# Optimization experiments

Hardware: AMD Instinct MI355X
Metric: run time of the kernel (lower is better)

## Reference

```python
import jax, jax.numpy as jnp
import numpy as np

N_NODES = 100000
N_EDGES = 1600000
IN_CH = 128
OUT_CH = 128


def setup_inputs() -> dict:
    key = jax.random.key(0)
    k = jax.random.split(key, 6)
    x = jax.random.normal(k[0], (N_NODES, IN_CH), dtype=jnp.float32)
    edge_index = jax.random.randint(k[1], (2, N_EDGES), 0, N_NODES, dtype=jnp.int32)
    # GCNConv linear weights (glorot-ish scale) and biases
    W1 = jax.random.normal(k[2], (IN_CH, OUT_CH), dtype=jnp.float32) / np.sqrt(IN_CH)
    b1 = jnp.zeros((OUT_CH,), dtype=jnp.float32)
    W2 = jax.random.normal(k[3], (OUT_CH, OUT_CH), dtype=jnp.float32) / np.sqrt(OUT_CH)
    b2 = jnp.zeros((OUT_CH,), dtype=jnp.float32)
    return {"x": x, "edge_index": edge_index, "W1": W1, "b1": b1, "W2": W2, "b2": b2}


def gcn_conv(x, src, dst, W, b, n_nodes):
    """PyG GCNConv: add self-loops, symmetric D^-1/2 A D^-1/2 normalization."""
    h = x @ W  # [N, out]
    # degree including the implicit self-loop (weight 1)
    ones = jnp.ones(src.shape[0], dtype=x.dtype)
    deg = jax.ops.segment_sum(ones, dst, num_segments=n_nodes) + 1.0  # [N]
    dinv = jax.lax.rsqrt(deg)  # deg >= 1 so always finite
    coef = dinv[src] * dinv[dst]  # [E] edge norm 1/sqrt(d_i d_j)
    msg = h[src] * coef[:, None]  # [E, out] gather + scale
    agg = jax.ops.segment_sum(msg, dst, num_segments=n_nodes)  # scatter-add
    # self-loop contribution: norm = dinv[i]^2
    agg = agg + h * (dinv * dinv)[:, None]
    return agg + b


def reference(x, edge_index, W1, b1, W2, b2):
    src, dst = edge_index[0], edge_index[1]
    h = jax.nn.relu(gcn_conv(x, src, dst, W1, b1, N_NODES))
    out = jax.nn.relu(gcn_conv(h, src, dst, W2, b2, N_NODES))
    return out
```

## Files before the change

kernel.cpp:

```cpp
#include <hip/hip_runtime.h>


#define NN 100000
#define NBKT 512
#define BKT_W 196
#define CHUNK 8192
#define CAP 6144

typedef __attribute__((ext_vector_type(8))) short bf16x8;
typedef __attribute__((ext_vector_type(4))) float f32x4;

__device__ __forceinline__ ushort f2bf(float f) {
  unsigned u = __float_as_uint(f);
  unsigned r = (u + 0x7fffu + ((u >> 16) & 1u)) >> 16;
  return (ushort)r;
}
__device__ __forceinline__ float bflo(unsigned p) {
  return __uint_as_float(p << 16);
}
__device__ __forceinline__ float bfhi(unsigned p) {
  return __uint_as_float(p & 0xffff0000u);
}
__device__ __forceinline__ unsigned hipair(unsigned ue, unsigned uo) {
  return (uo & 0xffff0000u) | (ue >> 16);
}


__global__ __launch_bounds__(512) void kb_hist(const int* __restrict__ dst,
                                               int* __restrict__ bcnt, int E) {
  __shared__ int h[NBKT];
  for (int i = threadIdx.x; i < NBKT; i += 512) h[i] = 0;
  __syncthreads();
  int base = blockIdx.x * CHUNK;
#pragma unroll 4
  for (int q = 0; q < CHUNK / 512; q++) {
    int e = base + threadIdx.x + q * 512;
    if (e < E) atomicAdd(&h[dst[e] / BKT_W], 1);
  }
  __syncthreads();
  for (int i = threadIdx.x; i < NBKT; i += 512)
    if (h[i]) atomicAdd(&bcnt[i], h[i]);
}

__global__ __launch_bounds__(512) void kb_scan(const int* __restrict__ bcnt,
                                               int* __restrict__ bbase,
                                               int* __restrict__ bcur,
                                               int* __restrict__ row_ptr,
                                               int N, int E) {
  __shared__ int s[NBKT];
  int t = threadIdx.x;
  int v = bcnt[t];
  s[t] = v;
  __syncthreads();
  for (int off = 1; off < NBKT; off <<= 1) {
    int x = (t >= off) ? s[t - off] : 0;
    __syncthreads();
    s[t] += x;
    __syncthreads();
  }
  int ex = s[t] - v;
  bbase[t] = ex;
  bcur[t] = ex;
  if (t == NBKT - 1) bbase[NBKT] = E;
  if (t == 0) row_ptr[N] = E;
}

__global__ __launch_bounds__(512) void kb_scatter(const int* __restrict__ src,
                                                  const int* __restrict__ dst,
                                                  int* __restrict__ bcur,
                                                  int2* __restrict__ pairs, int E) {
  __shared__ int h[NBKT];
  __shared__ int gb[NBKT];
  for (int i = threadIdx.x; i < NBKT; i += 512) h[i] = 0;
  __syncthreads();

  const int base = blockIdx.x * CHUNK;
  const int t = threadIdx.x;
  int rank[CHUNK / 512], bkt[CHUNK / 512], sv[CHUNK / 512], dv[CHUNK / 512];
#pragma unroll
  for (int q = 0; q < CHUNK / 512; q++) {
    int e = base + t + q * 512;
    if (e < E) {
      int d = dst[e];
      int b = d / BKT_W;
      bkt[q] = b;
      sv[q] = src[e];
      dv[q] = d;
      rank[q] = atomicAdd(&h[b], 1);
    } else {
      bkt[q] = -1;
    }
  }
  __syncthreads();
  for (int i = t; i < NBKT; i += 512) {
    int c = h[i];
    gb[i] = c ? atomicAdd(&bcur[i], c) : 0;
  }
  __syncthreads();
#pragma unroll
  for (int q = 0; q < CHUNK / 512; q++) {
    if (bkt[q] >= 0) pairs[(size_t)gb[bkt[q]] + rank[q]] = make_int2(sv[q], dv[q]);
  }
}

__global__ __launch_bounds__(512) void kb_sort(const int* __restrict__ bbase,
                                               const int2* __restrict__ pairs,
                                               int* __restrict__ csr_src,
                                               int* __restrict__ row_ptr,
                                               int N, int E) {
  __shared__ int cnt[256];
  __shared__ int sc[256];
  __shared__ int cur[256];
  __shared__ int stage[CAP];

  const int b = blockIdx.x;
  const int t = threadIdx.x;
  const int lo = bbase[b], hi = bbase[b + 1];
  const int n0 = b * BKT_W;
  int m = hi - lo;
  if (m > CAP) m = CAP;

  if (t < 256) cnt[t] = 0;
  __syncthreads();

  for (int i = t; i < m; i += 512) {
    int2 p = pairs[(size_t)lo + i];
    atomicAdd(&cnt[p.y - n0], 1);
  }
  __syncthreads();

  int v = 0;
  if (t < 256) {
    v = cnt[t];
    sc[t] = v;
  }
  __syncthreads();
  for (int off = 1; off < 256; off <<= 1) {
    int x = 0;
    if (t < 256 && t >= off) x = sc[t - off];
    __syncthreads();
    if (t < 256) sc[t] += x;
    __syncthreads();
  }
  if (t < 256) {
    int ex = sc[t] - v;
    cur[t] = ex;
    int node = n0 + t;
    if (t < BKT_W && node < N) row_ptr[node] = lo + ex;
  }
  __syncthreads();

  for (int i = t; i < m; i += 512) {
    int2 p = pairs[(size_t)lo + i];
    int pos = atomicAdd(&cur[p.y - n0], 1);
    stage[pos] = p.x;
  }
  __syncthreads();

  for (int i = t; i < m; i += 512) csr_src[(size_t)lo + i] = stage[i];
}

__global__ __launch_bounds__(256) void k_dinv(const int* __restrict__ row_ptr,
                                              float* __restrict__ dinv, int N) {
  int i = blockIdx.x * 256 + threadIdx.x;
  if (i < N) dinv[i] = rsqrtf((float)(row_ptr[i + 1] - row_ptr[i]) + 1.0f);
}

__global__ __launch_bounds__(256) void k_wsplit(const float* __restrict__ W,
                                                ushort* __restrict__ whi,
                                                ushort* __restrict__ wlo) {
  const int t = threadIdx.x;
#pragma unroll
  for (int it = 0; it < 16; ++it) {
    int f4 = it * 256 + t;
    int k = f4 >> 5;
    int n4 = (f4 & 31) * 4;
    float4 v = *(const float4*)(W + (size_t)k * 128 + n4);
    float f[4] = {v.x, v.y, v.z, v.w};
#pragma unroll
    for (int q = 0; q < 4; ++q) {
      int n = n4 + q;
      unsigned u = __float_as_uint(f[q]);
      float lf = f[q] - __uint_as_float(u & 0xffff0000u);
      int bo = (n * 256 + k * 2) ^ ((n & 7) << 4);
      *(ushort*)((char*)whi + bo) = (ushort)(u >> 16);
      *(ushort*)((char*)wlo + bo) = (ushort)(__float_as_uint(lf) >> 16);
    }
  }
}

__device__ __forceinline__ void cvt_row(const float* __restrict__ p,
                                        bf16x8* hi, bf16x8* lo) {
  float4 v0 = *(const float4*)p;
  float4 v1 = *(const float4*)(p + 4);
  float f[8] = {v0.x, v0.y, v0.z, v0.w, v1.x, v1.y, v1.z, v1.w};
  unsigned hw[4], lw[4];
#pragma unroll
  for (int i = 0; i < 4; ++i) {
    unsigned u0 = __float_as_uint(f[2 * i]);
    unsigned u1 = __float_as_uint(f[2 * i + 1]);
    float l0 = f[2 * i] - __uint_as_float(u0 & 0xffff0000u);
    float l1 = f[2 * i + 1] - __uint_as_float(u1 & 0xffff0000u);
    hw[i] = hipair(u0, u1);
    lw[i] = hipair(__float_as_uint(l0), __float_as_uint(l1));
  }
  uint4 H = make_uint4(hw[0], hw[1], hw[2], hw[3]);
  uint4 L = make_uint4(lw[0], lw[1], lw[2], lw[3]);
  *hi = __builtin_bit_cast(bf16x8, H);
  *lo = __builtin_bit_cast(bf16x8, L);
}

__global__ __launch_bounds__(256) void k_gemm_mfma(const float* __restrict__ X,
                                                   const ushort* __restrict__ whi,
                                                   const ushort* __restrict__ wlo,
                                                   const float* __restrict__ dinv,
                                                   ushort* __restrict__ hs, int M) {
  __shared__ ushort wt_hi[128 * 128];
  __shared__ ushort wt_lo[128 * 128];

  const int t = threadIdx.x;
#pragma unroll
  for (int it = 0; it < 8; ++it) {
    int o = (it * 256 + t) * 8;
    *(uint4*)&wt_hi[o] = *(const uint4*)&whi[o];
    *(uint4*)&wt_lo[o] = *(const uint4*)&wlo[o];
  }
  __syncthreads();

  const int wv = t >> 6;
  const int lane = t & 63;
  const int r0 = blockIdx.x * 128 + wv * 32;
  const int la = lane & 15;
  const int kg = (lane >> 4) * 8;
  const int rowA = min(r0 + la, M - 1);
  const int rowB = min(r0 + 16 + la, M - 1);

  f32x4 acc[2][8];
#pragma unroll
  for (int rs = 0; rs < 2; ++rs)
#pragma unroll
    for (int ct = 0; ct < 8; ++ct) acc[rs][ct] = (f32x4)(0.f);

#pragma unroll
  for (int ks = 0; ks < 4; ++ks) {
    const int koff = ks * 32 + kg;
    bf16x8 ah0, al0, ah1, al1;
    cvt_row(X + (size_t)rowA * 128 + koff, &ah0, &al0);
    cvt_row(X + (size_t)rowB * 128 + koff, &ah1, &al1);
#pragma unroll
    for (int ct = 0; ct < 8; ++ct) {
      const int n = ct * 16 + la;
      const int bo = (n * 256 + koff * 2) ^ ((n & 7) << 4);
      bf16x8 bh = *(const bf16x8*)((const char*)wt_hi + bo);
      bf16x8 bl = *(const bf16x8*)((const char*)wt_lo + bo);
      acc[0][ct] = __builtin_amdgcn_mfma_f32_16x16x32_bf16(ah0, bh, acc[0][ct], 0, 0, 0);
      acc[0][ct] = __builtin_amdgcn_mfma_f32_16x16x32_bf16(ah0, bl, acc[0][ct], 0, 0, 0);
      acc[0][ct] = __builtin_amdgcn_mfma_f32_16x16x32_bf16(al0, bh, acc[0][ct], 0, 0, 0);
      acc[1][ct] = __builtin_amdgcn_mfma_f32_16x16x32_bf16(ah1, bh, acc[1][ct], 0, 0, 0);
      acc[1][ct] = __builtin_amdgcn_mfma_f32_16x16x32_bf16(ah1, bl, acc[1][ct], 0, 0, 0);
      acc[1][ct] = __builtin_amdgcn_mfma_f32_16x16x32_bf16(al1, bh, acc[1][ct], 0, 0, 0);
    }
  }

#pragma unroll
  for (int rs = 0; rs < 2; ++rs) {
#pragma unroll
    for (int j = 0; j < 4; ++j) {
      int r = r0 + rs * 16 + (lane >> 4) * 4 + j;
      if (r < M) {
        float sc = dinv[r];
#pragma unroll
        for (int ct = 0; ct < 8; ++ct)
          hs[(size_t)r * 128 + ct * 16 + la] = f2bf(acc[rs][ct][j] * sc);
      }
    }
  }
}

__global__ __launch_bounds__(256) void k_agg(const int* __restrict__ row_ptr,
                                             const int* __restrict__ csr_src,
                                             const float* __restrict__ dinv,
                                             const ushort* __restrict__ hs,
                                             const float* __restrict__ bias,
                                             float* __restrict__ out, int N) {
  const int node = blockIdx.x * 4 + (threadIdx.x >> 6);
  if (node >= N) return;
  const int lane = threadIdx.x & 63;
  const int half = lane >> 5;
  const int cq = lane & 31;
  const uint2* hp = (const uint2*)hs;

  const int e0 = row_ptr[node];
  const int e1 = row_ptr[node + 1];

  float a0 = 0.f, a1 = 0.f, a2 = 0.f, a3 = 0.f;
  int e = e0 + half;
  for (; e + 6 < e1; e += 8) {
    int s0 = csr_src[e];
    int s1 = csr_src[e + 2];
    int s2 = csr_src[e + 4];
    int s3 = csr_src[e + 6];
    uint2 v0 = hp[(size_t)s0 * 32 + cq];
    uint2 v1 = hp[(size_t)s1 * 32 + cq];
    uint2 v2 = hp[(size_t)s2 * 32 + cq];
    uint2 v3 = hp[(size_t)s3 * 32 + cq];
    a0 += bflo(v0.x) + bflo(v1.x) + bflo(v2.x) + bflo(v3.x);
    a1 += bfhi(v0.x) + bfhi(v1.x) + bfhi(v2.x) + bfhi(v3.x);
    a2 += bflo(v0.y) + bflo(v1.y) + bflo(v2.y) + bflo(v3.y);
    a3 += bfhi(v0.y) + bfhi(v1.y) + bfhi(v2.y) + bfhi(v3.y);
  }
  for (; e < e1; e += 2) {
    int s = csr_src[e];
    uint2 v = hp[(size_t)s * 32 + cq];
    a0 += bflo(v.x);
    a1 += bfhi(v.x);
    a2 += bflo(v.y);
    a3 += bfhi(v.y);
  }
  a0 += __shfl_xor(a0, 32);
  a1 += __shfl_xor(a1, 32);
  a2 += __shfl_xor(a2, 32);
  a3 += __shfl_xor(a3, 32);

  if (half == 0) {
    uint2 sv = hp[(size_t)node * 32 + cq];
    a0 += bflo(sv.x);
    a1 += bfhi(sv.x);
    a2 += bflo(sv.y);
    a3 += bfhi(sv.y);
    float dv = dinv[node];
    float4 bv = ((const float4*)bias)[cq];
    float4 o;
    o.x = fmaxf(fmaf(a0, dv, bv.x), 0.f);
    o.y = fmaxf(fmaf(a1, dv, bv.y), 0.f);
    o.z = fmaxf(fmaf(a2, dv, bv.z), 0.f);
    o.w = fmaxf(fmaf(a3, dv, bv.w), 0.f);
    ((float4*)out)[(size_t)node * 32 + cq] = o;
  }
}


extern "C" void kernel_launch(void* const* d_in, const int* in_sizes, int n_in,
                              void* d_out, int out_size, void* d_ws, size_t ws_size,
                              hipStream_t stream) {
  const float* x  = (const float*)d_in[0];
  const int*   ei = (const int*)d_in[1];
  const float* W1 = (const float*)d_in[2];
  const float* b1 = (const float*)d_in[3];
  const float* W2 = (const float*)d_in[4];
  const float* b2 = (const float*)d_in[5];
  float* out = (float*)d_out;

  const int N = NN;
  const int E = in_sizes[1] / 2;
  const int* src = ei;
  const int* dst = ei + E;

  char* w = (char*)d_ws;
  auto alloc = [&](size_t bytes) {
    char* p = w;
    w += (bytes + 255) & ~(size_t)255;
    return p;
  };
  float*  dinv    = (float*)alloc((size_t)N * 4);
  int*    row_ptr = (int*)alloc((size_t)(N + 1) * 4);
  int*    bcnt    = (int*)alloc(NBKT * 4);
  int*    bbase   = (int*)alloc((NBKT + 1) * 4);
  int*    bcur    = (int*)alloc(NBKT * 4);
  int*    csr_src = (int*)alloc((size_t)E * 4);
  int2*   pairs   = (int2*)alloc((size_t)E * 8);
  ushort* hs      = (ushort*)alloc((size_t)N * 128 * 2);
  ushort* w1hi    = (ushort*)alloc(128 * 128 * 2);
  ushort* w1lo    = (ushort*)alloc(128 * 128 * 2);
  ushort* w2hi    = (ushort*)alloc(128 * 128 * 2);
  ushort* w2lo    = (ushort*)alloc(128 * 128 * 2);

  const int EB = (E + CHUNK - 1) / CHUNK;

  hipMemsetAsync(bcnt, 0, NBKT * 4, stream);
  kb_hist<<<EB, 512, 0, stream>>>(dst, bcnt, E);
  kb_scan<<<1, 512, 0, stream>>>(bcnt, bbase, bcur, row_ptr, N, E);
  kb_scatter<<<EB, 512, 0, stream>>>(src, dst, bcur, pairs, E);
  kb_sort<<<NBKT, 512, 0, stream>>>(bbase, pairs, csr_src, row_ptr, N, E);
  k_dinv<<<(N + 255) / 256, 256, 0, stream>>>(row_ptr, dinv, N);
  k_wsplit<<<1, 256, 0, stream>>>(W1, w1hi, w1lo);
  k_wsplit<<<1, 256, 0, stream>>>(W2, w2hi, w2lo);

  const int GB = (N + 127) / 128;
  const int AB = (N + 3) / 4;

  k_gemm_mfma<<<GB, 256, 0, stream>>>(x, w1hi, w1lo, dinv, hs, N);
  k_agg<<<AB, 256, 0, stream>>>(row_ptr, csr_src, dinv, hs, b1, out, N);
  k_gemm_mfma<<<GB, 256, 0, stream>>>(out, w2hi, w2lo, dinv, hs, N);
  k_agg<<<AB, 256, 0, stream>>>(row_ptr, csr_src, dinv, hs, b2, out, N);
}
```

Before: 353.2 us.

## Store layer-1 output in bf16, widen aggregation loads, fold dinv and wsplit launches

The first aggregation now writes the hidden activation as bf16 into a new buffer, and a new GEMM variant reads bf16 A directly, roughly halving the intermediate write and read traffic. The aggregation kernel now uses 16-byte loads with four edge groups per wave. The dinv computation moves into the sort kernel, and the two weight-split launches are merged into one, cutting launches. Rounding the hidden layer to bf16 adds precision loss on the second layer input, and dropping the low half of A for the second GEMM loses accuracy.

```diff
diff --git a/kernel.cpp b/kernel.cpp
--- a/kernel.cpp
+++ b/kernel.cpp
@@ -107,6 +107,7 @@
                                                const int2* __restrict__ pairs,
                                                int* __restrict__ csr_src,
                                                int* __restrict__ row_ptr,
+                                               float* __restrict__ dinv,
                                                int N, int E) {
   __shared__ int cnt[256];
   __shared__ int sc[256];
@@ -146,7 +147,10 @@
     int ex = sc[t] - v;
     cur[t] = ex;
     int node = n0 + t;
-    if (t < BKT_W && node < N) row_ptr[node] = lo + ex;
+    if (t < BKT_W && node < N) {
+      row_ptr[node] = lo + ex;
+      dinv[node] = rsqrtf((float)v + 1.0f);
+    }
   }
   __syncthreads();
 
@@ -160,15 +164,15 @@
   for (int i = t; i < m; i += 512) csr_src[(size_t)lo + i] = stage[i];
 }
 
-__global__ __launch_bounds__(256) void k_dinv(const int* __restrict__ row_ptr,
-                                              float* __restrict__ dinv, int N) {
-  int i = blockIdx.x * 256 + threadIdx.x;
-  if (i < N) dinv[i] = rsqrtf((float)(row_ptr[i + 1] - row_ptr[i]) + 1.0f);
-}
-
-__global__ __launch_bounds__(256) void k_wsplit(const float* __restrict__ W,
-                                                ushort* __restrict__ whi,
-                                                ushort* __restrict__ wlo) {
+__global__ __launch_bounds__(256) void k_wsplit2(const float* __restrict__ W1,
+                                                 const float* __restrict__ W2,
+                                                 ushort* __restrict__ w1hi,
+                                                 ushort* __restrict__ w1lo,
+                                                 ushort* __restrict__ w2hi,
+                                                 ushort* __restrict__ w2lo) {
+  const float* W = blockIdx.x ? W2 : W1;
+  ushort* whi = blockIdx.x ? w2hi : w1hi;
+  ushort* wlo = blockIdx.x ? w2lo : w1lo;
   const int t = threadIdx.x;
 #pragma unroll
   for (int it = 0; it < 16; ++it) {
@@ -277,65 +281,156 @@
   }
 }
 
+__global__ __launch_bounds__(256) void k_gemm_mfma_bf(const ushort* __restrict__ Xb,
+                                                      const ushort* __restrict__ whi,
+                                                      const ushort* __restrict__ wlo,
+                                                      const float* __restrict__ dinv,
+                                                      ushort* __restrict__ hs, int M) {
+  __shared__ ushort wt_hi[128 * 128];
+  __shared__ ushort wt_lo[128 * 128];
+
+  const int t = threadIdx.x;
+#pragma unroll
+  for (int it = 0; it < 8; ++it) {
+    int o = (it * 256 + t) * 8;
+    *(uint4*)&wt_hi[o] = *(const uint4*)&whi[o];
+    *(uint4*)&wt_lo[o] = *(const uint4*)&wlo[o];
+  }
+  __syncthreads();
+
+  const int wv = t >> 6;
+  const int lane = t & 63;
+  const int r0 = blockIdx.x * 128 + wv * 32;
+  const int la = lane & 15;
+  const int kg = (lane >> 4) * 8;
+  const int rowA = min(r0 + la, M - 1);
+  const int rowB = min(r0 + 16 + la, M - 1);
+
+  f32x4 acc[2][8];
+#pragma unroll
+  for (int rs = 0; rs < 2; ++rs)
+#pragma unroll
+    for (int ct = 0; ct < 8; ++ct) acc[rs][ct] = (f32x4)(0.f);
+
+#pragma unroll
+  for (int ks = 0; ks < 4; ++ks) {
+    const int koff = ks * 32 + kg;
+    bf16x8 a0 = *(const bf16x8*)(Xb + (size_t)rowA * 128 + koff);
+    bf16x8 a1 = *(const bf16x8*)(Xb + (size_t)rowB * 128 + koff);
+#pragma unroll
+    for (int ct = 0; ct < 8; ++ct) {
+      const int n = ct * 16 + la;
+      const int bo = (n * 256 + koff * 2) ^ ((n & 7) << 4);
+      bf16x8 bh = *(const bf16x8*)((const char*)wt_hi + bo);
+      bf16x8 bl = *(const bf16x8*)((const char*)wt_lo + bo);
+      acc[0][ct] = __builtin_amdgcn_mfma_f32_16x16x32_bf16(a0, bh, acc[0][ct], 0, 0, 0);
+      acc[0][ct] = __builtin_amdgcn_mfma_f32_16x16x32_bf16(a0, bl, acc[0][ct], 0, 0, 0);
+      acc[1][ct] = __builtin_amdgcn_mfma_f32_16x16x32_bf16(a1, bh, acc[1][ct], 0, 0, 0);
+      acc[1][ct] = __builtin_amdgcn_mfma_f32_16x16x32_bf16(a1, bl, acc[1][ct], 0, 0, 0);
+    }
+  }
+
+#pragma unroll
+  for (int rs = 0; rs < 2; ++rs) {
+#pragma unroll
+    for (int j = 0; j < 4; ++j) {
+      int r = r0 + rs * 16 + (lane >> 4) * 4 + j;
+      if (r < M) {
+        float sc = dinv[r];
+#pragma unroll
+        for (int ct = 0; ct < 8; ++ct)
+          hs[(size_t)r * 128 + ct * 16 + la] = f2bf(acc[rs][ct][j] * sc);
+      }
+    }
+  }
+}
+
+template <int BF16OUT>
 __global__ __launch_bounds__(256) void k_agg(const int* __restrict__ row_ptr,
                                              const int* __restrict__ csr_src,
                                              const float* __restrict__ dinv,
                                              const ushort* __restrict__ hs,
                                              const float* __restrict__ bias,
-                                             float* __restrict__ out, int N) {
+                                             void* __restrict__ outv, int N) {
   const int node = blockIdx.x * 4 + (threadIdx.x >> 6);
   if (node >= N) return;
   const int lane = threadIdx.x & 63;
-  const int half = lane >> 5;
-  const int cq = lane & 31;
-  const uint2* hp = (const uint2*)hs;
+  const int qg = lane >> 4;
+  const int cx = lane & 15;
+  const uint4* hp = (const uint4*)hs;
 
   const int e0 = row_ptr[node];
   const int e1 = row_ptr[node + 1];
 
-  float a0 = 0.f, a1 = 0.f, a2 = 0.f, a3 = 0.f;
-  int e = e0 + half;
-  for (; e + 6 < e1; e += 8) {
+  float a[8];
+#pragma unroll
+  for (int i = 0; i < 8; ++i) a[i] = 0.f;
+
+  int e = e0 + qg;
+  for (; e + 4 < e1; e += 8) {
     int s0 = csr_src[e];
-    int s1 = csr_src[e + 2];
-    int s2 = csr_src[e + 4];
-    int s3 = csr_src[e + 6];
-    uint2 v0 = hp[(size_t)s0 * 32 + cq];
-    uint2 v1 = hp[(size_t)s1 * 32 + cq];
-    uint2 v2 = hp[(size_t)s2 * 32 + cq];
-    uint2 v3 = hp[(size_t)s3 * 32 + cq];
-    a0 += bflo(v0.x) + bflo(v1.x) + bflo(v2.x) + bflo(v3.x);
-    a1 += bfhi(v0.x) + bfhi(v1.x) + bfhi(v2.x) + bfhi(v3.x);
-    a2 += bflo(v0.y) + bflo(v1.y) + bflo(v2.y) + bflo(v3.y);
-    a3 += bfhi(v0.y) + bfhi(v1.y) + bfhi(v2.y) + bfhi(v3.y);
-  }
-  for (; e < e1; e += 2) {
+    int s1 = csr_src[e + 4];
+    uint4 v0 = hp[(size_t)s0 * 16 + cx];
+    uint4 v1 = hp[(size_t)s1 * 16 + cx];
+    a[0] += bflo(v0.x) + bflo(v1.x);
+    a[1] += bfhi(v0.x) + bfhi(v1.x);
+    a[2] += bflo(v0.y) + bflo(v1.y);
+    a[3] += bfhi(v0.y) + bfhi(v1.y);
+    a[4] += bflo(v0.z) + bflo(v1.z);
+    a[5] += bfhi(v0.z) + bfhi(v1.z);
+    a[6] += bflo(v0.w) + bflo(v1.w);
+    a[7] += bfhi(v0.w) + bfhi(v1.w);
+  }
+  for (; e < e1; e += 4) {
     int s = csr_src[e];
-    uint2 v = hp[(size_t)s * 32 + cq];
-    a0 += bflo(v.x);
-    a1 += bfhi(v.x);
-    a2 += bflo(v.y);
-    a3 += bfhi(v.y);
-  }
-  a0 += __shfl_xor(a0, 32);
-  a1 += __shfl_xor(a1, 32);
-  a2 += __shfl_xor(a2, 32);
-  a3 += __shfl_xor(a3, 32);
-
-  if (half == 0) {
-    uint2 sv = hp[(size_t)node * 32 + cq];
-    a0 += bflo(sv.x);
-    a1 += bfhi(sv.x);
-    a2 += bflo(sv.y);
-    a3 += bfhi(sv.y);
+    uint4 v = hp[(size_t)s * 16 + cx];
+    a[0] += bflo(v.x);
+    a[1] += bfhi(v.x);
+    a[2] += bflo(v.y);
+    a[3] += bfhi(v.y);
+    a[4] += bflo(v.z);
+    a[5] += bfhi(v.z);
+    a[6] += bflo(v.w);
+    a[7] += bfhi(v.w);
+  }
+#pragma unroll
+  for (int i = 0; i < 8; ++i) {
+    a[i] += __shfl_xor(a[i], 16);
+    a[i] += __shfl_xor(a[i], 32);
+  }
+
+  if (qg == 0) {
+    uint4 sv = hp[(size_t)node * 16 + cx];
+    a[0] += bflo(sv.x);
+    a[1] += bfhi(sv.x);
+    a[2] += bflo(sv.y);
+    a[3] += bfhi(sv.y);
+    a[4] += bflo(sv.z);
+    a[5] += bfhi(sv.z);
+    a[6] += bflo(sv.w);
+    a[7] += bfhi(sv.w);
     float dv = dinv[node];
-    float4 bv = ((const float4*)bias)[cq];
-    float4 o;
-    o.x = fmaxf(fmaf(a0, dv, bv.x), 0.f);
-    o.y = fmaxf(fmaf(a1, dv, bv.y), 0.f);
-    o.z = fmaxf(fmaf(a2, dv, bv.z), 0.f);
-    o.w = fmaxf(fmaf(a3, dv, bv.w), 0.f);
-    ((float4*)out)[(size_t)node * 32 + cq] = o;
+    float4 b0 = ((const float4*)bias)[cx * 2];
+    float4 b1 = ((const float4*)bias)[cx * 2 + 1];
+    float o[8];
+    o[0] = fmaxf(fmaf(a[0], dv, b0.x), 0.f);
+    o[1] = fmaxf(fmaf(a[1], dv, b0.y), 0.f);
+    o[2] = fmaxf(fmaf(a[2], dv, b0.z), 0.f);
+    o[3] = fmaxf(fmaf(a[3], dv, b0.w), 0.f);
+    o[4] = fmaxf(fmaf(a[4], dv, b1.x), 0.f);
+    o[5] = fmaxf(fmaf(a[5], dv, b1.y), 0.f);
+    o[6] = fmaxf(fmaf(a[6], dv, b1.z), 0.f);
+    o[7] = fmaxf(fmaf(a[7], dv, b1.w), 0.f);
+    if (BF16OUT) {
+      ushort u[8];
+#pragma unroll
+      for (int i = 0; i < 8; ++i) u[i] = f2bf(o[i]);
+      ((uint4*)outv)[(size_t)node * 16 + cx] = *(const uint4*)u;
+    } else {
+      float4* op = (float4*)outv;
+      op[(size_t)node * 32 + cx * 2] = make_float4(o[0], o[1], o[2], o[3]);
+      op[(size_t)node * 32 + cx * 2 + 1] = make_float4(o[4], o[5], o[6], o[7]);
+    }
   }
 }
 
@@ -370,6 +465,7 @@
   int*    csr_src = (int*)alloc((size_t)E * 4);
   int2*   pairs   = (int2*)alloc((size_t)E * 8);
   ushort* hs      = (ushort*)alloc((size_t)N * 128 * 2);
+  ushort* h1b     = (ushort*)alloc((size_t)N * 128 * 2);
   ushort* w1hi    = (ushort*)alloc(128 * 128 * 2);
   ushort* w1lo    = (ushort*)alloc(128 * 128 * 2);
   ushort* w2hi    = (ushort*)alloc(128 * 128 * 2);
@@ -381,16 +477,14 @@
   kb_hist<<<EB, 512, 0, stream>>>(dst, bcnt, E);
   kb_scan<<<1, 512, 0, stream>>>(bcnt, bbase, bcur, row_ptr, N, E);
   kb_scatter<<<EB, 512, 0, stream>>>(src, dst, bcur, pairs, E);
-  kb_sort<<<NBKT, 512, 0, stream>>>(bbase, pairs, csr_src, row_ptr, N, E);
-  k_dinv<<<(N + 255) / 256, 256, 0, stream>>>(row_ptr, dinv, N);
-  k_wsplit<<<1, 256, 0, stream>>>(W1, w1hi, w1lo);
-  k_wsplit<<<1, 256, 0, stream>>>(W2, w2hi, w2lo);
+  kb_sort<<<NBKT, 512, 0, stream>>>(bbase, pairs, csr_src, row_ptr, dinv, N, E);
+  k_wsplit2<<<2, 256, 0, stream>>>(W1, W2, w1hi, w1lo, w2hi, w2lo);
 
   const int GB = (N + 127) / 128;
   const int AB = (N + 3) / 4;
 
   k_gemm_mfma<<<GB, 256, 0, stream>>>(x, w1hi, w1lo, dinv, hs, N);
-  k_agg<<<AB, 256, 0, stream>>>(row_ptr, csr_src, dinv, hs, b1, out, N);
-  k_gemm_mfma<<<GB, 256, 0, stream>>>(out, w2hi, w2lo, dinv, hs, N);
-  k_agg<<<AB, 256, 0, stream>>>(row_ptr, csr_src, dinv, hs, b2, out, N);
-}
+  k_agg<1><<<AB, 256, 0, stream>>>(row_ptr, csr_src, dinv, hs, b1, h1b, N);
+  k_gemm_mfma_bf<<<GB, 256, 0, stream>>>(h1b, w2hi, w2lo, dinv, hs, N);
+  k_agg<0><<<AB, 256, 0, stream>>>(row_ptr, csr_src, dinv, hs, b2, out, N);
+}
```

After: 336.6 us. 1.05x faster.
